# Performance work log

Measured on AMD Instinct MI355X. Metric: run time of the kernel, lower is better.

Reference implementation:

```python
import jax, jax.numpy as jnp
import numpy as np

CH3 = np.array([[0,1,2],[1,2,3],[2,3,4],[3,4,5],[0,4,5],[0,1,5]])  # [6,3]
CH4 = np.array([[0,1,2,3],[1,2,3,4],[2,3,4,5],[0,3,4,5],[0,1,4,5],
                [0,1,2,5],[0,1,3,4],[1,2,4,5],[0,2,3,5]])          # [9,4]
K = 5

def setup_inputs() -> dict:
    key = jax.random.key(0)
    ks = jax.random.split(key, 8)
    x  = jax.random.normal(ks[0], (32, 6, 512, 512), dtype=jnp.float32)
    # params, scaled like torch default kaiming-uniform-ish (bound = 1/sqrt(fan_in))
    def u(k, shape, fan_in):
        b = 1.0 / np.sqrt(fan_in)
        return jax.random.uniform(k, shape, jnp.float32, -b, b)
    w3 = u(ks[1], (6, 3, K, K), 3 * K * K)
    b3 = u(ks[2], (6,), 3 * K * K)
    w4 = u(ks[3], (9, 4, K, K), 4 * K * K)
    b4 = u(ks[4], (9,), 4 * K * K)
    w6 = u(ks[5], (1, 6, K, K), 6 * K * K)
    b6 = u(ks[6], (1,), 6 * K * K)
    return {"x": x, "w3": w3, "b3": b3, "w4": w4, "b4": b4, "w6": w6, "b6": b6}

def _full_kernel(w3, w4, w6):
    # Scatter the per-subset filters into one [16,6,5,5] OIHW kernel; unused
    # input channels stay zero, which is mathematically identical to gathering
    # channel subsets per the original module.
    W = jnp.zeros((16, 6, K, K), dtype=w3.dtype)
    W = W.at[jnp.arange(6)[:, None], CH3].set(w3)
    W = W.at[(6 + jnp.arange(9))[:, None], CH4].set(w4)
    W = W.at[15].set(w6[0])
    return W

def reference(x, w3, b3, w4, b4, w6, b6):
    Wfull = _full_kernel(w3, w4, w6)
    bias = jnp.concatenate([b3, b4, b6])  # [16]
    out = jax.lax.conv_general_dilated(
        x, Wfull, window_strides=(1, 1), padding='VALID',
        dimension_numbers=('NCHW', 'OIHW', 'NCHW'))
    return out + bias[None, :, None, None]  # [B,16,H-4,W-4]
```

## Files before the change

### kernel.cpp

```cpp
#include <hip/hip_runtime.h>


#define OW 508
#define BX 64
#define BY 16
#define TC 68
#define NS 20

typedef _Float16 h8 __attribute__((ext_vector_type(8)));
typedef _Float16 h2 __attribute__((ext_vector_type(2)));
typedef float f32x16 __attribute__((ext_vector_type(16)));

__device__ __constant__ int d_CH3[6][3] = {
    {0,1,2},{1,2,3},{2,3,4},{3,4,5},{0,4,5},{0,1,5}};
__device__ __constant__ int d_CH4[9][4] = {
    {0,1,2,3},{1,2,3,4},{2,3,4,5},{0,3,4,5},{0,1,4,5},
    {0,1,2,5},{0,1,3,4},{1,2,4,5},{0,2,3,5}};

__global__ void prep_weights(const float* __restrict__ w3, const float* __restrict__ b3,
                             const float* __restrict__ w4, const float* __restrict__ b4,
                             const float* __restrict__ w6, const float* __restrict__ b6,
                             float* __restrict__ bias, unsigned short* __restrict__ AF) {
    __shared__ float Wfull[16 * 6 * 25];
    const int tid = threadIdx.x;
    for (int i = tid; i < 16 * 6 * 25; i += 256) Wfull[i] = 0.f;
    __syncthreads();
    for (int i = tid; i < 6 * 3 * 25; i += 256) {
        int oc = i / 75, r = i % 75, c = r / 25, t = r % 25;
        Wfull[(oc * 6 + d_CH3[oc][c]) * 25 + t] = w3[i];
    }
    for (int i = tid; i < 9 * 4 * 25; i += 256) {
        int o = i / 100, r = i % 100, c = r / 25, t = r % 25;
        Wfull[((6 + o) * 6 + d_CH4[o][c]) * 25 + t] = w4[i];
    }
    for (int i = tid; i < 6 * 25; i += 256) Wfull[15 * 150 + i] = w6[i];
    __syncthreads();
    for (int i = tid; i < 15 * 64 * 8; i += 256) {
        int e = i & 7, lane = (i >> 3) & 63, q = i >> 9;
        int kx = q / 3, ch = q % 3;
        int oc = lane & 15, dy = (lane >> 4) & 1, rr = lane >> 5;
        int ky = ch * 2 + rr - dy;
        float w = 0.f;
        if (e < 6 && ky >= 0 && ky <= 4) w = Wfull[(oc * 6 + e) * 25 + ky * 5 + kx];
        _Float16 hw = (_Float16)w;
        AF[i] = __builtin_bit_cast(unsigned short, hw);
    }
    if (tid < 6)        bias[tid] = b3[tid];
    else if (tid < 15)  bias[tid] = b4[tid - 6];
    else if (tid == 15) bias[tid] = b6[0];
}

__global__ __launch_bounds__(256, 4) void conv_mfma(
        const float* __restrict__ x, const unsigned short* __restrict__ AF,
        const float* __restrict__ bias, float* __restrict__ out) {
    __shared__ uint4 T4[NS * TC];

    const int tid = threadIdx.x;

    const int id  = blockIdx.x + 8 * (blockIdx.y + 32 * blockIdx.z);
    const int xcd = id & 7;
    const int pos = id >> 3;
    const int bz  = xcd * 4 + (pos >> 8);
    const int r_  = pos & 255;
    const int by  = r_ >> 3;
    const int bx  = r_ & 7;

    const int gx0 = bx * BX;
    const int oy0 = by * BY;
    const float* xb = x + (size_t)bz * 6 * 512 * 512;

    const int lane = tid & 63;
    const int h = lane >> 5;

    h8 afr[15];
    #pragma unroll
    for (int q = 0; q < 15; ++q)
        afr[q] = *reinterpret_cast<const h8*>(AF + (q * 64 + lane) * 8);

    f32x16 binit;
    #pragma unroll
    for (int reg = 0; reg < 16; ++reg)
        binit[reg] = bias[((reg & 3) + 8 * ((reg >> 2) & 1) + 4 * h) & 15];

    #pragma unroll
    for (int k = 0; k < 3; ++k) {
        int idx = tid + k * 256;
        if (idx < 34 * NS) {
            int cp = idx % 34;
            int rr = idx / 34;
            int c = 2 * cp, gx = gx0 + c, gy = oy0 + rr;
            float2 v[6];
            #pragma unroll
            for (int ic = 0; ic < 6; ++ic) v[ic] = (float2){0.f, 0.f};
            if (gy < 512 && gx < 512) {
                const float* rp = xb + (size_t)gy * 512 + gx;
                #pragma unroll
                for (int ic = 0; ic < 6; ++ic)
                    v[ic] = *(const float2*)(rp + (size_t)ic * 262144);
            }
            h2 a0; a0.x = (_Float16)v[0].x; a0.y = (_Float16)v[1].x;
            h2 a1; a1.x = (_Float16)v[2].x; a1.y = (_Float16)v[3].x;
            h2 a2; a2.x = (_Float16)v[4].x; a2.y = (_Float16)v[5].x;
            h2 b0; b0.x = (_Float16)v[0].y; b0.y = (_Float16)v[1].y;
            h2 b1; b1.x = (_Float16)v[2].y; b1.y = (_Float16)v[3].y;
            h2 b2; b2.x = (_Float16)v[4].y; b2.y = (_Float16)v[5].y;
            uint4 wA, wB;
            wA.x = __builtin_bit_cast(unsigned int, a0);
            wA.y = __builtin_bit_cast(unsigned int, a1);
            wA.z = __builtin_bit_cast(unsigned int, a2);
            wA.w = 0u;
            wB.x = __builtin_bit_cast(unsigned int, b0);
            wB.y = __builtin_bit_cast(unsigned int, b1);
            wB.z = __builtin_bit_cast(unsigned int, b2);
            wB.w = 0u;
            T4[rr * TC + c]     = wA;
            T4[rr * TC + c + 1] = wB;
        }
    }
    __syncthreads();

    const int wv = tid >> 6;
    const int s  = wv & 1;
    const int dh = wv >> 1;
    const int colb = s * 32 + (lane & 31);
    const int px = gx0 + colb;
    const bool pxok = (px < OW);
    const size_t cs = (size_t)OW * OW;
    float* ob = out + ((size_t)bz * 16 + 4 * h) * cs + px;

    #pragma unroll 1
    for (int dd = 0; dd < 8; dd += 4) {
        const int d0 = dh * 8 + dd;
        f32x16 accA = binit;
        f32x16 accB = binit;
        #pragma unroll
        for (int kx = 0; kx < 5; ++kx) {
            const uint4* cb = &T4[(d0 + h) * TC + colb + kx];
            h8 b0 = *reinterpret_cast<const h8*>(&cb[0]);
            h8 b1 = *reinterpret_cast<const h8*>(&cb[2 * TC]);
            h8 b2 = *reinterpret_cast<const h8*>(&cb[4 * TC]);
            h8 b3 = *reinterpret_cast<const h8*>(&cb[6 * TC]);
            accA = __builtin_amdgcn_mfma_f32_32x32x16_f16(afr[kx * 3 + 0], b0, accA, 0, 0, 0);
            accB = __builtin_amdgcn_mfma_f32_32x32x16_f16(afr[kx * 3 + 0], b1, accB, 0, 0, 0);
            accA = __builtin_amdgcn_mfma_f32_32x32x16_f16(afr[kx * 3 + 1], b1, accA, 0, 0, 0);
            accB = __builtin_amdgcn_mfma_f32_32x32x16_f16(afr[kx * 3 + 1], b2, accB, 0, 0, 0);
            accA = __builtin_amdgcn_mfma_f32_32x32x16_f16(afr[kx * 3 + 2], b2, accA, 0, 0, 0);
            accB = __builtin_amdgcn_mfma_f32_32x32x16_f16(afr[kx * 3 + 2], b3, accB, 0, 0, 0);
        }
        #pragma unroll
        for (int dy = 0; dy < 2; ++dy) {
            #pragma unroll
            for (int r8 = 0; r8 < 8; ++r8) {
                const int reg = dy * 8 + r8;
                const int ocb = (r8 & 3) + 8 * (r8 >> 2);
                const int oyA = oy0 + d0 + dy;
                const int oyB = oyA + 2;
                if (oyA < OW && pxok)
                    ob[(size_t)ocb * cs + (size_t)oyA * OW] = accA[reg];
                if (oyB < OW && pxok)
                    ob[(size_t)ocb * cs + (size_t)oyB * OW] = accB[reg];
            }
        }
    }
}

extern "C" void kernel_launch(void* const* d_in, const int* in_sizes, int n_in,
                              void* d_out, int out_size, void* d_ws, size_t ws_size,
                              hipStream_t stream) {
    const float* x  = (const float*)d_in[0];
    const float* w3 = (const float*)d_in[1];
    const float* b3 = (const float*)d_in[2];
    const float* w4 = (const float*)d_in[3];
    const float* b4 = (const float*)d_in[4];
    const float* w6 = (const float*)d_in[5];
    const float* b6 = (const float*)d_in[6];
    float* out = (float*)d_out;

    float* bias        = (float*)d_ws;
    unsigned short* AF = (unsigned short*)(bias + 16);

    prep_weights<<<1, 256, 0, stream>>>(w3, b3, w4, b4, w6, b6, bias, AF);

    dim3 grid(8, 32, 32);
    conv_mfma<<<grid, 256, 0, stream>>>(x, AF, bias, out);
}
```

Measured before the change: 242.4 us.

## Stream input rows through a shared-memory ring buffer with taller 512-thread blocks

Each block now covers 32 output rows with 512 threads, keeping a 32-row ring buffer of packed fp16 input rows in LDS. Eight new rows are loaded per step while MFMA work runs on resident rows, then written into the ring after compute. This reduces redundant halo loads and lets global loads overlap compute. It adds a barrier per step and lowers grid parallelism.

```diff
diff --git a/kernel.cpp b/kernel.cpp
--- a/kernel.cpp
+++ b/kernel.cpp
@@ -3,9 +3,8 @@
 
 #define OW 508
 #define BX 64
-#define BY 16
 #define TC 68
-#define NS 20
+#define RM 31
 
 typedef _Float16 h8 __attribute__((ext_vector_type(8)));
 typedef _Float16 h2 __attribute__((ext_vector_type(2)));
@@ -50,23 +49,39 @@
     else if (tid == 15) bias[tid] = b6[0];
 }
 
-__global__ __launch_bounds__(256, 4) void conv_mfma(
+__device__ __forceinline__ void pack2(const float2 (&v)[6], uint4& wA, uint4& wB) {
+    h2 a0; a0.x = (_Float16)v[0].x; a0.y = (_Float16)v[1].x;
+    h2 a1; a1.x = (_Float16)v[2].x; a1.y = (_Float16)v[3].x;
+    h2 a2; a2.x = (_Float16)v[4].x; a2.y = (_Float16)v[5].x;
+    h2 b0; b0.x = (_Float16)v[0].y; b0.y = (_Float16)v[1].y;
+    h2 b1; b1.x = (_Float16)v[2].y; b1.y = (_Float16)v[3].y;
+    h2 b2; b2.x = (_Float16)v[4].y; b2.y = (_Float16)v[5].y;
+    wA.x = __builtin_bit_cast(unsigned int, a0);
+    wA.y = __builtin_bit_cast(unsigned int, a1);
+    wA.z = __builtin_bit_cast(unsigned int, a2);
+    wA.w = 0u;
+    wB.x = __builtin_bit_cast(unsigned int, b0);
+    wB.y = __builtin_bit_cast(unsigned int, b1);
+    wB.z = __builtin_bit_cast(unsigned int, b2);
+    wB.w = 0u;
+}
+
+__global__ __launch_bounds__(512, 4) void conv_mfma(
         const float* __restrict__ x, const unsigned short* __restrict__ AF,
         const float* __restrict__ bias, float* __restrict__ out) {
-    __shared__ uint4 T4[NS * TC];
+    __shared__ uint4 T4[32 * TC];
 
     const int tid = threadIdx.x;
 
-    const int id  = blockIdx.x + 8 * (blockIdx.y + 32 * blockIdx.z);
+    const int id  = blockIdx.x + 8 * (blockIdx.y + 16 * blockIdx.z);
     const int xcd = id & 7;
     const int pos = id >> 3;
-    const int bz  = xcd * 4 + (pos >> 8);
-    const int r_  = pos & 255;
-    const int by  = r_ >> 3;
-    const int bx  = r_ & 7;
+    const int bz  = xcd * 4 + (pos >> 7);
+    const int by  = (pos >> 3) & 15;
+    const int bx  = pos & 7;
 
     const int gx0 = bx * BX;
-    const int oy0 = by * BY;
+    const int Y0  = by * 32;
     const float* xb = x + (size_t)bz * 6 * 512 * 512;
 
     const int lane = tid & 63;
@@ -77,42 +92,28 @@
     for (int q = 0; q < 15; ++q)
         afr[q] = *reinterpret_cast<const h8*>(AF + (q * 64 + lane) * 8);
 
-    f32x16 binit;
+    float bv[8];
     #pragma unroll
-    for (int reg = 0; reg < 16; ++reg)
-        binit[reg] = bias[((reg & 3) + 8 * ((reg >> 2) & 1) + 4 * h) & 15];
+    for (int r8 = 0; r8 < 8; ++r8)
+        bv[r8] = bias[(r8 & 3) + 8 * (r8 >> 2) + 4 * h];
 
     #pragma unroll
-    for (int k = 0; k < 3; ++k) {
-        int idx = tid + k * 256;
-        if (idx < 34 * NS) {
-            int cp = idx % 34;
-            int rr = idx / 34;
-            int c = 2 * cp, gx = gx0 + c, gy = oy0 + rr;
+    for (int k = 0; k < 2; ++k) {
+        int idx = tid + k * 512;
+        if (idx < 680) {
+            int cp = idx % 34, rr = idx / 34;
+            int c = 2 * cp, gx = gx0 + c, gy = Y0 + rr;
             float2 v[6];
             #pragma unroll
             for (int ic = 0; ic < 6; ++ic) v[ic] = (float2){0.f, 0.f};
-            if (gy < 512 && gx < 512) {
+            if (gx < 512) {
                 const float* rp = xb + (size_t)gy * 512 + gx;
                 #pragma unroll
                 for (int ic = 0; ic < 6; ++ic)
                     v[ic] = *(const float2*)(rp + (size_t)ic * 262144);
             }
-            h2 a0; a0.x = (_Float16)v[0].x; a0.y = (_Float16)v[1].x;
-            h2 a1; a1.x = (_Float16)v[2].x; a1.y = (_Float16)v[3].x;
-            h2 a2; a2.x = (_Float16)v[4].x; a2.y = (_Float16)v[5].x;
-            h2 b0; b0.x = (_Float16)v[0].y; b0.y = (_Float16)v[1].y;
-            h2 b1; b1.x = (_Float16)v[2].y; b1.y = (_Float16)v[3].y;
-            h2 b2; b2.x = (_Float16)v[4].y; b2.y = (_Float16)v[5].y;
             uint4 wA, wB;
-            wA.x = __builtin_bit_cast(unsigned int, a0);
-            wA.y = __builtin_bit_cast(unsigned int, a1);
-            wA.z = __builtin_bit_cast(unsigned int, a2);
-            wA.w = 0u;
-            wB.x = __builtin_bit_cast(unsigned int, b0);
-            wB.y = __builtin_bit_cast(unsigned int, b1);
-            wB.z = __builtin_bit_cast(unsigned int, b2);
-            wB.w = 0u;
+            pack2(v, wA, wB);
             T4[rr * TC + c]     = wA;
             T4[rr * TC + c + 1] = wB;
         }
@@ -121,7 +122,8 @@
 
     const int wv = tid >> 6;
     const int s  = wv & 1;
-    const int dh = wv >> 1;
+    const int dh = (wv >> 1) & 1;
+    const int ch = wv >> 2;
     const int colb = s * 32 + (lane & 31);
     const int px = gx0 + colb;
     const bool pxok = (px < OW);
@@ -129,38 +131,59 @@
     float* ob = out + ((size_t)bz * 16 + 4 * h) * cs + px;
 
     #pragma unroll 1
-    for (int dd = 0; dd < 8; dd += 4) {
-        const int d0 = dh * 8 + dd;
-        f32x16 accA = binit;
-        f32x16 accB = binit;
+    for (int t = 0; t < 4; ++t) {
+        float2 va[6];
+        int wslot = -1, wcol = 0;
+        if (tid < 272) {
+            int cp = tid % 34, rr = tid / 34;
+            int c = 2 * cp, gx = gx0 + c, gy = Y0 + 8 * t + 20 + rr;
+            #pragma unroll
+            for (int ic = 0; ic < 6; ++ic) va[ic] = (float2){0.f, 0.f};
+            if (gy < 512 && gx < 512) {
+                const float* rp = xb + (size_t)gy * 512 + gx;
+                #pragma unroll
+                for (int ic = 0; ic < 6; ++ic)
+                    va[ic] = *(const float2*)(rp + (size_t)ic * 262144);
+            }
+            wslot = gy & RM;
+            wcol = c;
+        }
+
+        const int sb = 8 * t + 4 * dh + 2 * ch + h;
+        const int s0 = sb & RM, s1 = (sb + 2) & RM, s2 = (sb + 4) & RM;
+        f32x16 acc;
+        #pragma unroll
+        for (int r = 0; r < 16; ++r) acc[r] = 0.f;
         #pragma unroll
         for (int kx = 0; kx < 5; ++kx) {
-            const uint4* cb = &T4[(d0 + h) * TC + colb + kx];
-            h8 b0 = *reinterpret_cast<const h8*>(&cb[0]);
-            h8 b1 = *reinterpret_cast<const h8*>(&cb[2 * TC]);
-            h8 b2 = *reinterpret_cast<const h8*>(&cb[4 * TC]);
-            h8 b3 = *reinterpret_cast<const h8*>(&cb[6 * TC]);
-            accA = __builtin_amdgcn_mfma_f32_32x32x16_f16(afr[kx * 3 + 0], b0, accA, 0, 0, 0);
-            accB = __builtin_amdgcn_mfma_f32_32x32x16_f16(afr[kx * 3 + 0], b1, accB, 0, 0, 0);
-            accA = __builtin_amdgcn_mfma_f32_32x32x16_f16(afr[kx * 3 + 1], b1, accA, 0, 0, 0);
-            accB = __builtin_amdgcn_mfma_f32_32x32x16_f16(afr[kx * 3 + 1], b2, accB, 0, 0, 0);
-            accA = __builtin_amdgcn_mfma_f32_32x32x16_f16(afr[kx * 3 + 2], b2, accA, 0, 0, 0);
-            accB = __builtin_amdgcn_mfma_f32_32x32x16_f16(afr[kx * 3 + 2], b3, accB, 0, 0, 0);
-        }
+            h8 b0 = *reinterpret_cast<const h8*>(&T4[s0 * TC + colb + kx]);
+            h8 b1 = *reinterpret_cast<const h8*>(&T4[s1 * TC + colb + kx]);
+            h8 b2 = *reinterpret_cast<const h8*>(&T4[s2 * TC + colb + kx]);
+            acc = __builtin_amdgcn_mfma_f32_32x32x16_f16(afr[kx * 3 + 0], b0, acc, 0, 0, 0);
+            acc = __builtin_amdgcn_mfma_f32_32x32x16_f16(afr[kx * 3 + 1], b1, acc, 0, 0, 0);
+            acc = __builtin_amdgcn_mfma_f32_32x32x16_f16(afr[kx * 3 + 2], b2, acc, 0, 0, 0);
+        }
+
+        const int oyb = Y0 + 8 * t + 4 * dh + 2 * ch;
         #pragma unroll
         for (int dy = 0; dy < 2; ++dy) {
-            #pragma unroll
-            for (int r8 = 0; r8 < 8; ++r8) {
-                const int reg = dy * 8 + r8;
-                const int ocb = (r8 & 3) + 8 * (r8 >> 2);
-                const int oyA = oy0 + d0 + dy;
-                const int oyB = oyA + 2;
-                if (oyA < OW && pxok)
-                    ob[(size_t)ocb * cs + (size_t)oyA * OW] = accA[reg];
-                if (oyB < OW && pxok)
-                    ob[(size_t)ocb * cs + (size_t)oyB * OW] = accB[reg];
+            const int oy = oyb + dy;
+            if (oy < OW && pxok) {
+                #pragma unroll
+                for (int r8 = 0; r8 < 8; ++r8) {
+                    const int ocb = (r8 & 3) + 8 * (r8 >> 2);
+                    ob[(size_t)ocb * cs + (size_t)oy * OW] = acc[dy * 8 + r8] + bv[r8];
+                }
             }
         }
+
+        if (wslot >= 0) {
+            uint4 wA, wB;
+            pack2(va, wA, wB);
+            T4[wslot * TC + wcol]     = wA;
+            T4[wslot * TC + wcol + 1] = wB;
+        }
+        __syncthreads();
     }
 }
 
@@ -181,6 +204,6 @@
 
     prep_weights<<<1, 256, 0, stream>>>(w3, b3, w4, b4, w6, b6, bias, AF);
 
-    dim3 grid(8, 32, 32);
-    conv_mfma<<<grid, 256, 0, stream>>>(x, AF, bias, out);
-}
+    dim3 grid(8, 16, 32);
+    conv_mfma<<<grid, 512, 0, stream>>>(x, AF, bias, out);
+}
```

New measurement: 227.0 us. 6.3% less time.
